# Optimization experiments

Hardware: AMD Instinct MI355X
Metric: run time of the kernel (lower is better)

The kernel has to match this reference:

```python
import jax, jax.numpy as jnp
import numpy as np


def setup_inputs() -> dict:
    key = jax.random.key(0)
    ks = jax.random.split(key, 9)
    B, LAT, OBS, HID = 4096, 128, 64, 1024
    s = 0.05  # keep tanh out of full saturation
    return {
        "z": jax.random.normal(ks[0], (B, LAT), jnp.float32),
        "W_l2h": jax.random.normal(ks[1], (HID, LAT), jnp.float32) * s,
        "b_l2h": jax.random.normal(ks[2], (HID,), jnp.float32) * s,
        "W_ih": jax.random.normal(ks[3], (HID, OBS), jnp.float32) * s,
        "b_ih": jax.random.normal(ks[4], (HID,), jnp.float32) * s,
        "W_hh": jax.random.normal(ks[5], (HID, HID), jnp.float32) * s,
        "b_hh": jax.random.normal(ks[6], (HID,), jnp.float32) * s,
        "W_ho": jax.random.normal(ks[7], (OBS, HID), jnp.float32) * s,
        "b_ho": jax.random.normal(ks[8], (OBS,), jnp.float32) * s,
        "seq_len": 70,
    }


def reference(z, W_l2h, b_l2h, W_ih, b_ih, W_hh, b_hh, W_ho, b_ho, seq_len):
    B = z.shape[0]
    obs_dim = W_ho.shape[0]
    # latent -> initial hidden state (nn.Linear)
    h0 = z @ W_l2h.T + b_l2h                         # [B, HID]
    x0 = jnp.zeros((B, obs_dim), dtype=z.dtype)      # first RNN input is zeros

    def step(carry, _):
        h, x = carry
        # tanh RNN cell: h' = tanh(x W_ih^T + b_ih + h W_hh^T + b_hh)
        h = jnp.tanh(x @ W_ih.T + b_ih + h @ W_hh.T + b_hh)
        y = h @ W_ho.T + b_ho                        # output projection [B, OBS]
        x_next = jax.lax.stop_gradient(y)
        return (h, x_next), y

    _, ys = jax.lax.scan(step, (h0, x0), None, length=seq_len)  # [T, B, OBS]
    return jnp.transpose(ys, (1, 0, 2))              # [B, T, OBS]
```

## Files before the change

### kernel.cpp

```cpp
#include <hip/hip_runtime.h>
#include <hip/hip_bf16.h>
#include <stdint.h>

typedef _Float16 f16;
typedef _Float16 f16x8 __attribute__((ext_vector_type(8)));
typedef float f32x4 __attribute__((ext_vector_type(4)));

#define B_SZ 4096
#define HID  1024
#define LAT  128
#define OBS  64
#define TSEQ 70
#define SPLIT_SCALE 2048.0f
#define SPLIT_INV   (1.0f / 2048.0f)

__device__ __forceinline__ size_t tidx(int row, int k, int K) {
  return (size_t)((row >> 4) * (K >> 5) + (k >> 5)) * 512
       + ((k >> 3) & 3) * 128 + (row & 15) * 8 + (k & 7);
}

__device__ __forceinline__ void gl2lds16(const void* g, void* l) {
  __builtin_amdgcn_global_load_lds(
      (const __attribute__((address_space(1))) void*)g,
      (__attribute__((address_space(3))) void*)l, 16, 0, 0);
}

__device__ __forceinline__ float tanh_fast(float x) {
  float e = __expf(2.0f * x);
  return 1.0f - 2.0f / (e + 1.0f);
}

__global__ __launch_bounds__(256, 2) void rnn_step_split(
    const f16* __restrict__ Ah, const f16* __restrict__ Al,
    const f16* __restrict__ Wh, const f16* __restrict__ Wl,
    const float* __restrict__ bias,
    f16* __restrict__ Hh, f16* __restrict__ Hl, int K)
{
  __shared__ __align__(16) f16 sAh[16 * 512];
  __shared__ __align__(16) f16 sAl[16 * 512];
  __shared__ __align__(16) f16 sWh[8 * 512];
  __shared__ __align__(16) f16 sWl[8 * 512];

  const int lane = threadIdx.x & 63;
  const int wave = threadIdx.x >> 6;
  const int bm = blockIdx.x;
  const int bn = blockIdx.y;
  const int lo8 = lane * 8;
  const int kc = K >> 5;

  f32x4 acc0[2][4], acc1[2][4];
  const f32x4 z4 = {0.f, 0.f, 0.f, 0.f};
#pragma unroll
  for (int i = 0; i < 2; ++i)
#pragma unroll
    for (int j = 0; j < 4; ++j) { acc0[i][j] = z4; acc1[i][j] = z4; }

  const int nk = K >> 6;

  for (int it = 0; it < nk; ++it) {
#pragma unroll
    for (int u = 0; u < 2; ++u) {
      const int rg = wave * 2 + u;
#pragma unroll
      for (int s = 0; s < 2; ++s) {
        const size_t ga = (size_t)((bm * 8 + rg) * kc + (it * 2 + s)) * 512 + lo8;
        gl2lds16(Ah + ga, &sAh[(rg * 2 + s) * 512]);
        gl2lds16(Al + ga, &sAl[(rg * 2 + s) * 512]);
      }
    }
#pragma unroll
    for (int u = 0; u < 2; ++u) {
      const int c = wave * 2 + u;
      const int nrg = c >> 1, s = c & 1;
      const size_t gw = (size_t)((bn * 4 + nrg) * kc + (it * 2 + s)) * 512 + lo8;
      gl2lds16(Wh + gw, &sWh[c * 512]);
      gl2lds16(Wl + gw, &sWl[c * 512]);
    }
    __syncthreads();

#pragma unroll
    for (int s = 0; s < 2; ++s) {
      f16x8 vah[2], val[2], vwh[4], vwl[4];
#pragma unroll
      for (int i = 0; i < 2; ++i) {
        vah[i] = *(const f16x8*)&sAh[((wave * 2 + i) * 2 + s) * 512 + lo8];
        val[i] = *(const f16x8*)&sAl[((wave * 2 + i) * 2 + s) * 512 + lo8];
      }
#pragma unroll
      for (int j = 0; j < 4; ++j) {
        vwh[j] = *(const f16x8*)&sWh[(j * 2 + s) * 512 + lo8];
        vwl[j] = *(const f16x8*)&sWl[(j * 2 + s) * 512 + lo8];
      }
#pragma unroll
      for (int i = 0; i < 2; ++i)
#pragma unroll
        for (int j = 0; j < 4; ++j) {
          acc0[i][j] = __builtin_amdgcn_mfma_f32_16x16x32_f16(vah[i], vwh[j], acc0[i][j], 0, 0, 0);
          acc1[i][j] = __builtin_amdgcn_mfma_f32_16x16x32_f16(vah[i], vwl[j], acc1[i][j], 0, 0, 0);
          acc1[i][j] = __builtin_amdgcn_mfma_f32_16x16x32_f16(val[i], vwh[j], acc1[i][j], 0, 0, 0);
        }
    }
    __syncthreads();
  }

  const int rq = lane >> 4;
  const int cl = lane & 15;
#pragma unroll
  for (int j = 0; j < 4; ++j) {
    const int gcol = bn * 64 + j * 16 + cl;
    const float bb = bias[gcol];
#pragma unroll
    for (int i = 0; i < 2; ++i) {
      const int grow = bm * 128 + wave * 32 + i * 16 + rq * 4;
#pragma unroll
      for (int r = 0; r < 4; ++r) {
        const float a = acc0[i][j][r] + acc1[i][j][r] * SPLIT_INV + bb;
        const float t = tanh_fast(a);
        const f16 hi = (f16)t;
        const size_t idx = tidx(grow + r, gcol, HID);
        Hh[idx] = hi;
        Hl[idx] = (f16)((t - (float)hi) * SPLIT_SCALE);
      }
    }
  }
}

__global__ __launch_bounds__(256, 2) void proj_kernel(
    const f16* __restrict__ H, const f16* __restrict__ Who,
    const float* __restrict__ bho, float* __restrict__ Y, int t0)
{
  __shared__ __align__(16) f16 As[128 * 64];
  __shared__ __align__(16) f16 Bs[64 * 64];
  const int lane = threadIdx.x & 63;
  const int wave = threadIdx.x >> 6;
  const int bm = blockIdx.x;
  const int lo8 = lane * 8;

  f32x4 acc[2][4];
  const f32x4 z4 = {0.f, 0.f, 0.f, 0.f};
#pragma unroll
  for (int i = 0; i < 2; ++i)
#pragma unroll
    for (int j = 0; j < 4; ++j) acc[i][j] = z4;

  for (int kt = 0; kt < HID; kt += 64) {
    const int kch = kt >> 5;
#pragma unroll
    for (int u = 0; u < 4; ++u) {
      const int cidx = wave * 4 + u;
      const int mt = cidx >> 1, s = cidx & 1;
      gl2lds16(H + (size_t)((bm * 8 + mt) * 32 + kch + s) * 512 + lo8, &As[cidx * 512]);
    }
#pragma unroll
    for (int u = 0; u < 2; ++u) {
      const int cidx = wave * 2 + u;
      const int nt = cidx >> 1, s = cidx & 1;
      gl2lds16(Who + (size_t)(nt * 32 + kch + s) * 512 + lo8, &Bs[cidx * 512]);
    }
    __syncthreads();
#pragma unroll
    for (int s = 0; s < 2; ++s) {
      f16x8 af[2], bfr[4];
#pragma unroll
      for (int i = 0; i < 2; ++i)
        af[i] = *(const f16x8*)&As[(((wave * 2 + i) << 1) | s) * 512 + lo8];
#pragma unroll
      for (int j = 0; j < 4; ++j)
        bfr[j] = *(const f16x8*)&Bs[((j << 1) | s) * 512 + lo8];
#pragma unroll
      for (int i = 0; i < 2; ++i)
#pragma unroll
        for (int j = 0; j < 4; ++j)
          acc[i][j] = __builtin_amdgcn_mfma_f32_16x16x32_f16(af[i], bfr[j], acc[i][j], 0, 0, 0);
    }
    __syncthreads();
  }

  const int rq = lane >> 4;
  const int cl = lane & 15;
#pragma unroll
  for (int j = 0; j < 4; ++j) {
    const int col = j * 16 + cl;
    const float bb = bho[col];
#pragma unroll
    for (int i = 0; i < 2; ++i)
#pragma unroll
      for (int r = 0; r < 4; ++r) {
        const int row = bm * 128 + wave * 32 + i * 16 + rq * 4 + r;
        const int t = t0 + (row >> 12);
        const int b = row & 4095;
        Y[((size_t)b * TSEQ + t) * OBS + col] = acc[i][j][r] + bb;
      }
  }
}

__global__ void cast_tiled_kernel(const float* __restrict__ x, f16* __restrict__ y,
                                  int K, int n) {
  int i = blockIdx.x * blockDim.x + threadIdx.x;
  if (i < n) y[tidx(i / K, i % K, K)] = (f16)x[i];
}

__global__ void split_tiled_kernel(const float* __restrict__ x, f16* __restrict__ hi,
                                   f16* __restrict__ lo, int K, int n) {
  int i = blockIdx.x * blockDim.x + threadIdx.x;
  if (i < n) {
    float v = x[i];
    f16 h = (f16)v;
    size_t o = tidx(i / K, i % K, K);
    hi[o] = h;
    lo[o] = (f16)((v - (float)h) * SPLIT_SCALE);
  }
}

__global__ void prep_weff(const float* __restrict__ Whh, const float* __restrict__ Wih,
                          const float* __restrict__ Who,
                          f16* __restrict__ Wh, f16* __restrict__ Wl) {
  const int n = blockIdx.x;
  __shared__ float wih_row[OBS];
  if (threadIdx.x < OBS) wih_row[threadIdx.x] = Wih[n * OBS + threadIdx.x];
  __syncthreads();
  for (int k = threadIdx.x; k < HID; k += 256) {
    float s = Whh[(size_t)n * HID + k];
#pragma unroll 8
    for (int o = 0; o < OBS; ++o) s = fmaf(wih_row[o], Who[(size_t)o * HID + k], s);
    const size_t idx = tidx(n, k, HID);
    f16 h = (f16)s;
    Wh[idx] = h;
    Wl[idx] = (f16)((s - (float)h) * SPLIT_SCALE);
  }
}

__global__ void prep_w1(const float* __restrict__ Whh, const float* __restrict__ Wl2h,
                        f16* __restrict__ W1h, f16* __restrict__ W1l) {
  const int n = blockIdx.x, j = threadIdx.x;
  float s = 0.f;
  for (int k = 0; k < HID; ++k) s = fmaf(Whh[(size_t)n * HID + k], Wl2h[(size_t)k * LAT + j], s);
  const size_t idx = tidx(n, j, LAT);
  f16 h = (f16)s;
  W1h[idx] = h;
  W1l[idx] = (f16)((s - (float)h) * SPLIT_SCALE);
}

__global__ void prep_bias(const float* __restrict__ bih, const float* __restrict__ bhh,
                          const float* __restrict__ bho, const float* __restrict__ Wih,
                          const float* __restrict__ Whh, const float* __restrict__ bl2h,
                          float* __restrict__ beff, float* __restrict__ b1) {
  const int n = blockIdx.x, l = threadIdx.x;
  float s1 = Wih[(size_t)n * OBS + l] * bho[l];
  float s2 = 0.f;
  for (int k = l; k < HID; k += 64) s2 = fmaf(Whh[(size_t)n * HID + k], bl2h[k], s2);
#pragma unroll
  for (int off = 32; off > 0; off >>= 1) {
    s1 += __shfl_down(s1, off);
    s2 += __shfl_down(s2, off);
  }
  if (l == 0) {
    const float base = bih[n] + bhh[n];
    beff[n] = base + s1;
    b1[n]   = base + s2;
  }
}

extern "C" void kernel_launch(void* const* d_in, const int* in_sizes, int n_in,
                              void* d_out, int out_size, void* d_ws, size_t ws_size,
                              hipStream_t stream) {
  (void)in_sizes; (void)n_in; (void)out_size; (void)ws_size;
  const float* z    = (const float*)d_in[0];
  const float* Wl2h = (const float*)d_in[1];
  const float* bl2h = (const float*)d_in[2];
  const float* Wih  = (const float*)d_in[3];
  const float* bih  = (const float*)d_in[4];
  const float* Whh  = (const float*)d_in[5];
  const float* bhh  = (const float*)d_in[6];
  const float* Who  = (const float*)d_in[7];
  const float* bho  = (const float*)d_in[8];
  float* Y = (float*)d_out;

  char* ws = (char*)d_ws;
  size_t off = 0;
  auto take = [&](size_t bytes) {
    char* p = ws + off;
    off = (off + bytes + 255) & ~(size_t)255;
    return p;
  };
  f16*   Weffh = (f16*)take((size_t)HID * HID * 2);
  f16*   Weffl = (f16*)take((size_t)HID * HID * 2);
  f16*   W1h   = (f16*)take((size_t)HID * LAT * 2);
  f16*   W1l   = (f16*)take((size_t)HID * LAT * 2);
  f16*   Whob  = (f16*)take((size_t)OBS * HID * 2);
  f16*   zh    = (f16*)take((size_t)B_SZ * LAT * 2);
  f16*   zl    = (f16*)take((size_t)B_SZ * LAT * 2);
  float* beff  = (float*)take(HID * 4);
  float* b1    = (float*)take(HID * 4);

  const size_t S = (size_t)B_SZ * HID;
  f16* Hlo  = (f16*)take(2 * S * 2);
  f16* ring = (f16*)take(8 * S * 2);

  split_tiled_kernel<<<(B_SZ * LAT) / 256, 256, 0, stream>>>(z, zh, zl, LAT, B_SZ * LAT);
  cast_tiled_kernel<<<(OBS * HID) / 256, 256, 0, stream>>>(Who, Whob, HID, OBS * HID);
  prep_weff<<<HID, 256, 0, stream>>>(Whh, Wih, Who, Weffh, Weffl);
  prep_w1<<<HID, LAT, 0, stream>>>(Whh, Wl2h, W1h, W1l);
  prep_bias<<<HID, 64, 0, stream>>>(bih, bhh, bho, Wih, Whh, bl2h, beff, b1);

  dim3 sgrid(B_SZ / 128, HID / 64);
  rnn_step_split<<<sgrid, 256, 0, stream>>>(zh, zl, W1h, W1l, b1, ring, Hlo, LAT);
  for (int t = 1; t < TSEQ; ++t) {
    if ((t & 7) == 0)
      proj_kernel<<<(8 * B_SZ) / 128, 256, 0, stream>>>(ring, Whob, bho, Y, t - 8);
    rnn_step_split<<<sgrid, 256, 0, stream>>>(
        ring + (size_t)((t - 1) & 7) * S, Hlo + (size_t)((t - 1) & 1) * S,
        Weffh, Weffl, beff,
        ring + (size_t)(t & 7) * S, Hlo + (size_t)(t & 1) * S, HID);
  }
  proj_kernel<<<(6 * B_SZ) / 128, 256, 0, stream>>>(ring, Whob, bho, Y, 64);
}
```

Measured before the change: 2.468 ms.

## Pipeline split-f16 RNN step GEMM with a three-slot LDS ring buffer

Replaces the single-buffered K loop (64 per iteration, two barriers) with a three-slot LDS ring holding 32-wide K chunks. The next chunk's direct global-to-LDS loads are issued before computing the current one, with a vmcnt wait and a single barrier per iteration. This is meant to overlap memory latency with MFMA work and cut barrier count. In exchange it uses more LDS (72 KB per block), which may limit occupancy under the two-blocks-per-CU launch bound, and correctness depends on the exact vmcnt(6) counting.

```diff
diff --git a/kernel.cpp b/kernel.cpp
--- a/kernel.cpp
+++ b/kernel.cpp
@@ -36,10 +36,7 @@
     const float* __restrict__ bias,
     f16* __restrict__ Hh, f16* __restrict__ Hl, int K)
 {
-  __shared__ __align__(16) f16 sAh[16 * 512];
-  __shared__ __align__(16) f16 sAl[16 * 512];
-  __shared__ __align__(16) f16 sWh[8 * 512];
-  __shared__ __align__(16) f16 sWl[8 * 512];
+  __shared__ __align__(16) f16 ring[3][24 * 512];
 
   const int lane = threadIdx.x & 63;
   const int wave = threadIdx.x >> 6;
@@ -55,53 +52,56 @@
 #pragma unroll
     for (int j = 0; j < 4; ++j) { acc0[i][j] = z4; acc1[i][j] = z4; }
 
-  const int nk = K >> 6;
-
-  for (int it = 0; it < nk; ++it) {
+  auto stage = [&](int it, int slot) {
+    f16* b = ring[slot];
 #pragma unroll
     for (int u = 0; u < 2; ++u) {
       const int rg = wave * 2 + u;
-#pragma unroll
-      for (int s = 0; s < 2; ++s) {
-        const size_t ga = (size_t)((bm * 8 + rg) * kc + (it * 2 + s)) * 512 + lo8;
-        gl2lds16(Ah + ga, &sAh[(rg * 2 + s) * 512]);
-        gl2lds16(Al + ga, &sAl[(rg * 2 + s) * 512]);
+      const size_t ga = (size_t)((bm * 8 + rg) * kc + it) * 512 + lo8;
+      gl2lds16(Ah + ga, b + rg * 512);
+      gl2lds16(Al + ga, b + (8 + rg) * 512);
+    }
+    const size_t gw = (size_t)((bn * 4 + wave) * kc + it) * 512 + lo8;
+    gl2lds16(Wh + gw, b + (16 + wave) * 512);
+    gl2lds16(Wl + gw, b + (20 + wave) * 512);
+  };
+
+  auto compute = [&](int slot) {
+    const f16* b = ring[slot];
+    f16x8 vah[2], val[2], vwh[4], vwl[4];
+#pragma unroll
+    for (int i = 0; i < 2; ++i) {
+      vah[i] = *(const f16x8*)&b[(wave * 2 + i) * 512 + lo8];
+      val[i] = *(const f16x8*)&b[(8 + wave * 2 + i) * 512 + lo8];
+    }
+#pragma unroll
+    for (int j = 0; j < 4; ++j) {
+      vwh[j] = *(const f16x8*)&b[(16 + j) * 512 + lo8];
+      vwl[j] = *(const f16x8*)&b[(20 + j) * 512 + lo8];
+    }
+#pragma unroll
+    for (int i = 0; i < 2; ++i)
+#pragma unroll
+      for (int j = 0; j < 4; ++j) {
+        acc0[i][j] = __builtin_amdgcn_mfma_f32_16x16x32_f16(vah[i], vwh[j], acc0[i][j], 0, 0, 0);
+        acc1[i][j] = __builtin_amdgcn_mfma_f32_16x16x32_f16(vah[i], vwl[j], acc1[i][j], 0, 0, 0);
+        acc1[i][j] = __builtin_amdgcn_mfma_f32_16x16x32_f16(val[i], vwh[j], acc1[i][j], 0, 0, 0);
       }
-    }
-#pragma unroll
-    for (int u = 0; u < 2; ++u) {
-      const int c = wave * 2 + u;
-      const int nrg = c >> 1, s = c & 1;
-      const size_t gw = (size_t)((bn * 4 + nrg) * kc + (it * 2 + s)) * 512 + lo8;
-      gl2lds16(Wh + gw, &sWh[c * 512]);
-      gl2lds16(Wl + gw, &sWl[c * 512]);
-    }
-    __syncthreads();
-
-#pragma unroll
-    for (int s = 0; s < 2; ++s) {
-      f16x8 vah[2], val[2], vwh[4], vwl[4];
-#pragma unroll
-      for (int i = 0; i < 2; ++i) {
-        vah[i] = *(const f16x8*)&sAh[((wave * 2 + i) * 2 + s) * 512 + lo8];
-        val[i] = *(const f16x8*)&sAl[((wave * 2 + i) * 2 + s) * 512 + lo8];
-      }
-#pragma unroll
-      for (int j = 0; j < 4; ++j) {
-        vwh[j] = *(const f16x8*)&sWh[(j * 2 + s) * 512 + lo8];
-        vwl[j] = *(const f16x8*)&sWl[(j * 2 + s) * 512 + lo8];
-      }
-#pragma unroll
-      for (int i = 0; i < 2; ++i)
-#pragma unroll
-        for (int j = 0; j < 4; ++j) {
-          acc0[i][j] = __builtin_amdgcn_mfma_f32_16x16x32_f16(vah[i], vwh[j], acc0[i][j], 0, 0, 0);
-          acc1[i][j] = __builtin_amdgcn_mfma_f32_16x16x32_f16(vah[i], vwl[j], acc1[i][j], 0, 0, 0);
-          acc1[i][j] = __builtin_amdgcn_mfma_f32_16x16x32_f16(val[i], vwh[j], acc1[i][j], 0, 0, 0);
-        }
-    }
-    __syncthreads();
-  }
+  };
+
+  stage(0, 0);
+  int cur = 0;
+  for (int it = 0; it + 1 < kc; ++it) {
+    const int nxt = (cur == 2) ? 0 : cur + 1;
+    stage(it + 1, nxt);
+    asm volatile("s_waitcnt vmcnt(6)" ::: "memory");
+    __builtin_amdgcn_s_barrier();
+    compute(cur);
+    cur = nxt;
+  }
+  asm volatile("s_waitcnt vmcnt(0)" ::: "memory");
+  __builtin_amdgcn_s_barrier();
+  compute(cur);
 
   const int rq = lane >> 4;
   const int cl = lane & 15;
```

Measured after the change: 2.180 ms. 1.13x faster.
